# Performance work log

Hardware: AMD Instinct MI355X
Metric: run time of the kernel (lower is better)

## Reference

```python
import jax, jax.numpy as jnp
import numpy as np

D_MODEL = 1024
N_HEADS = 4  # hardcoded in the torch reshape
EPS = 1e-5


def setup_inputs() -> dict:
    key = jax.random.key(0)
    ks = jax.random.split(key, 5)
    d = D_MODEL
    x = jax.random.normal(ks[0], (4, 2048, d), dtype=jnp.float32)
    scale = 1.0 / np.sqrt(d)
    qkv_w = jax.random.normal(ks[1], (3 * d, d), dtype=jnp.float32) * scale
    qkv_b = jnp.zeros((3 * d,), dtype=jnp.float32)
    wo_w = jax.random.normal(ks[2], (d, d), dtype=jnp.float32) * scale
    wo_b = jnp.zeros((d,), dtype=jnp.float32)
    gamma = jnp.ones((d,), dtype=jnp.float32)
    beta = jnp.zeros((d,), dtype=jnp.float32)
    return {"x": x, "qkv_w": qkv_w, "qkv_b": qkv_b, "wo_w": wo_w,
            "wo_b": wo_b, "gamma": gamma, "beta": beta}


def reference(x, qkv_w, qkv_b, wo_w, wo_b, gamma, beta):
    b, s, d = x.shape
    h = N_HEADS
    hd = d // h
    # QKV projection (torch Linear: x @ W.T + b)
    qkv = x @ qkv_w.T + qkv_b                      # [b, s, 3d]
    qkv = qkv.reshape(b, s, 3, h, hd)
    qkv = jnp.transpose(qkv, (2, 0, 3, 1, 4))      # [3, b, h, s, hd]
    q, k, v = qkv[0], qkv[1], qkv[2]
    scores = jnp.einsum('bhqd,bhkd->bhqk', q, k) * (hd ** -0.5)
    attn = jax.nn.softmax(scores, axis=-1)
    out = jnp.einsum('bhqk,bhkd->bhqd', attn, v)   # [b, h, s, hd]
    out = jnp.transpose(out, (0, 2, 1, 3)).reshape(b, s, d)
    y = x + (out @ wo_w.T + wo_b)
    # LayerNorm over last dim
    mu = jnp.mean(y, axis=-1, keepdims=True)
    var = jnp.var(y, axis=-1, keepdims=True)
    return (y - mu) * jax.lax.rsqrt(var + EPS) * gamma + beta
```

## Files before the change

### kernel.cpp

```cpp
#include <hip/hip_runtime.h>
#include <hip/hip_bf16.h>

#define SEQ 2048
#define DM  1024
#define NH  4
#define HD  256

typedef __attribute__((ext_vector_type(4))) float f32x4;
typedef __attribute__((ext_vector_type(16))) float f32x16;
typedef __attribute__((ext_vector_type(8))) short bf16x8;

__device__ __forceinline__ void gload16(const void* g, void* l) {
  __builtin_amdgcn_global_load_lds(
      (__attribute__((address_space(1))) void*)(unsigned long long)(g),
      (__attribute__((address_space(3))) void*)(l), 16, 0, 0);
}

__device__ __forceinline__ bf16x8 ldg8(const __hip_bfloat16* p) {
  return *reinterpret_cast<const bf16x8*>(p);
}

__device__ __forceinline__ unsigned pack2(float a, float b) {
  __hip_bfloat162 t = __float22bfloat162_rn(make_float2(a, b));
  return *reinterpret_cast<unsigned*>(&t);
}

__device__ __forceinline__ short bfbits(float x) {
  __hip_bfloat16 h = __float2bfloat16(x);
  return *reinterpret_cast<short*>(&h);
}

__global__ __launch_bounds__(256) void cvt_f32_bf16(const float* __restrict__ in,
                                                    __hip_bfloat16* __restrict__ out, int n4) {
  int i = blockIdx.x * 256 + threadIdx.x;
  if (i >= n4) return;
  float4 v = reinterpret_cast<const float4*>(in)[i];
  __hip_bfloat162* o2 = reinterpret_cast<__hip_bfloat162*>(out);
  o2[i * 2 + 0] = __float22bfloat162_rn(make_float2(v.x, v.y));
  o2[i * 2 + 1] = __float22bfloat162_rn(make_float2(v.z, v.w));
}

template <int EPI>
__global__ __launch_bounds__(256, 2) void gemm_bt(
    const __hip_bfloat16* __restrict__ A, const __hip_bfloat16* __restrict__ Bw,
    const float* __restrict__ bias, const float* __restrict__ resid,
    __hip_bfloat16* __restrict__ Cb, float* __restrict__ Cf, int M, int N, int K) {
  __shared__ __hip_bfloat16 ldsA[128 * 32];
  __shared__ __hip_bfloat16 ldsB[128 * 32];
  const int t = threadIdx.x;
  const int w = t >> 6, l = t & 63;
  const int lg = l >> 4, li = l & 15;
  const int m0 = blockIdx.y * 128, n0 = blockIdx.x * 128;
  const int wm = (w >> 1) * 64, wn = (w & 1) * 64;
  const int c1 = t + 256;
  const __hip_bfloat16* gA0 = A + (size_t)(m0 + (t >> 2)) * K + (t & 3) * 8;
  const __hip_bfloat16* gA1 = A + (size_t)(m0 + (c1 >> 2)) * K + (c1 & 3) * 8;
  const __hip_bfloat16* gB0 = Bw + (size_t)(n0 + (t >> 2)) * K + (t & 3) * 8;
  const __hip_bfloat16* gB1 = Bw + (size_t)(n0 + (c1 >> 2)) * K + (c1 & 3) * 8;
  __hip_bfloat16* lA0 = ldsA + t * 8;
  __hip_bfloat16* lA1 = ldsA + c1 * 8;
  __hip_bfloat16* lB0 = ldsB + t * 8;
  __hip_bfloat16* lB1 = ldsB + c1 * 8;
  f32x4 acc[4][4] = {};
  for (int k0 = 0; k0 < K; k0 += 32) {
    gload16(gA0 + k0, lA0);
    gload16(gA1 + k0, lA1);
    gload16(gB0 + k0, lB0);
    gload16(gB1 + k0, lB1);
    __syncthreads();
    bf16x8 af[4], bfr[4];
#pragma unroll
    for (int i = 0; i < 4; i++) af[i] = ldg8(&ldsA[(wm + i * 16 + li) * 32 + lg * 8]);
#pragma unroll
    for (int i = 0; i < 4; i++) bfr[i] = ldg8(&ldsB[(wn + i * 16 + li) * 32 + lg * 8]);
#pragma unroll
    for (int mi = 0; mi < 4; mi++)
#pragma unroll
      for (int ni = 0; ni < 4; ni++)
        acc[mi][ni] = __builtin_amdgcn_mfma_f32_16x16x32_bf16(af[mi], bfr[ni], acc[mi][ni], 0, 0, 0);
    __syncthreads();
  }
#pragma unroll
  for (int ni = 0; ni < 4; ni++) {
    const int col = n0 + wn + ni * 16 + li;
    const float bv = bias[col];
#pragma unroll
    for (int mi = 0; mi < 4; mi++) {
      const int rowb = m0 + wm + mi * 16 + lg * 4;
#pragma unroll
      for (int r = 0; r < 4; r++) {
        const size_t idx = (size_t)(rowb + r) * N + col;
        float v = acc[mi][ni][r] + bv;
        if (EPI) {
          Cf[idx] = v + resid[idx];
        } else {
          Cb[idx] = __float2bfloat16(v);
        }
      }
    }
  }
}

__global__ __launch_bounds__(256) void transpose_v(const short* __restrict__ qkv,
                                                   short* __restrict__ vt) {
  __shared__ short tile[32][36];
  const int t = threadIdx.x;
  const int bh = blockIdx.z, b = bh >> 2, h = bh & 3;
  const int s0 = blockIdx.x * 32, d0 = blockIdx.y * 32;
  const int sr = t >> 3, c4 = (t & 7) * 4;
  const short* src = qkv + (size_t)(b * SEQ + s0 + sr) * 3072 + 2048 + h * HD + d0 + c4;
  short4 vv = *reinterpret_cast<const short4*>(src);
  tile[sr][c4 + 0] = vv.x;
  tile[sr][c4 + 1] = vv.y;
  tile[sr][c4 + 2] = vv.z;
  tile[sr][c4 + 3] = vv.w;
  __syncthreads();
  short* dst = vt + (size_t)(bh * HD + d0 + sr) * SEQ + s0 + c4;
  short4 ov;
  ov.x = tile[c4 + 0][sr];
  ov.y = tile[c4 + 1][sr];
  ov.z = tile[c4 + 2][sr];
  ov.w = tile[c4 + 3][sr];
  *reinterpret_cast<short4*>(dst) = ov;
}

__global__ __launch_bounds__(512, 2) void flash_attn(const __hip_bfloat16* __restrict__ qkv,
                                                     const __hip_bfloat16* __restrict__ vt,
                                                     __hip_bfloat16* __restrict__ attno) {
  __shared__ __hip_bfloat16 ldsK[2][2][32 * 256];
  __shared__ __hip_bfloat16 ldsV[2][2][256 * 32];
  __shared__ float mlx[8][2][32];
  const int tid = threadIdx.x, w = tid >> 6, l = tid & 63;
  const int l31 = l & 31, hi = l >> 5;
  const int g = w >> 2, gt = tid & 255;
  const int bid = blockIdx.x;
  const int bh = (bid & 7) * 2 + ((bid >> 3) & 1);
  const int qt = bid >> 4;
  const int b = bh >> 2, h = bh & 3;
  const int qsub = qt * 128 + (w & 3) * 32;
  const int kvbase = g * 1024;
  bf16x8 bq[16];
  {
    const __hip_bfloat16* Qp = qkv + (size_t)(b * SEQ + qsub + l31) * 3072 + h * HD + hi * 8;
#pragma unroll
    for (int kst = 0; kst < 16; kst++) bq[kst] = ldg8(Qp + kst * 16);
  }
  const int kcd = (gt & 31) ^ ((gt >> 5) & 7);
  const __hip_bfloat16* Kg =
      qkv + (size_t)(b * SEQ + kvbase + (gt >> 5)) * 3072 + 1024 + h * HD + kcd * 8;
  const int vcd = (gt & 3) ^ ((gt >> 3) & 3);
  const __hip_bfloat16* Vg =
      vt + (size_t)bh * HD * SEQ + (size_t)(gt >> 2) * SEQ + kvbase + vcd * 8;
  __hip_bfloat16* lKb[2] = {&ldsK[g][0][0], &ldsK[g][1][0]};
  __hip_bfloat16* lVb[2] = {&ldsV[g][0][0], &ldsV[g][1][0]};

  f32x16 oacc[8] = {};
  float m_run = -1e30f, lsum = 0.f;

#pragma unroll
  for (int i = 0; i < 4; i++) gload16(Kg + (size_t)(i * 8) * 3072, lKb[0] + i * 2048 + gt * 8);
#pragma unroll
  for (int i = 0; i < 4; i++) gload16(Vg + (size_t)(i * 64) * SEQ, lVb[0] + i * 2048 + gt * 8);
  __syncthreads();

#pragma unroll 2
  for (int t = 0; t < 32; ++t) {
    const int cur = t & 1;
    if (t + 1 < 32) {
      const int nk = (t + 1) * 32;
#pragma unroll
      for (int i = 0; i < 4; i++)
        gload16(Kg + (size_t)(nk + i * 8) * 3072, lKb[cur ^ 1] + i * 2048 + gt * 8);
#pragma unroll
      for (int i = 0; i < 4; i++)
        gload16(Vg + (size_t)(i * 64) * SEQ + nk, lVb[cur ^ 1] + i * 2048 + gt * 8);
    }
    const __hip_bfloat16* lK = lKb[cur];
    const __hip_bfloat16* lV = lVb[cur];
    f32x16 sa = {}, sb = {};
    const int ksw = l31 & 7;
    __builtin_amdgcn_s_setprio(1);
#pragma unroll
    for (int kst = 0; kst < 8; kst++) {
      bf16x8 aka = ldg8(&lK[l31 * 256 + (((4 * kst + hi) ^ ksw) << 3)]);
      bf16x8 akb = ldg8(&lK[l31 * 256 + (((4 * kst + 2 + hi) ^ ksw) << 3)]);
      sa = __builtin_amdgcn_mfma_f32_32x32x16_bf16(aka, bq[2 * kst], sa, 0, 0, 0);
      sb = __builtin_amdgcn_mfma_f32_32x32x16_bf16(akb, bq[2 * kst + 1], sb, 0, 0, 0);
    }
    __builtin_amdgcn_s_setprio(0);
#pragma unroll
    for (int r = 0; r < 16; r++) sa[r] = (sa[r] + sb[r]) * 0.0625f;
    float rmax = sa[0];
#pragma unroll
    for (int r = 1; r < 16; r++) rmax = fmaxf(rmax, sa[r]);
    rmax = fmaxf(rmax, __shfl_xor(rmax, 32));
    if (rmax > m_run + 8.f) {
      const float alpha = __expf(m_run - rmax);
      m_run = rmax;
      lsum *= alpha;
#pragma unroll
      for (int dt = 0; dt < 8; dt++)
#pragma unroll
        for (int r = 0; r < 16; r++) oacc[dt][r] *= alpha;
    }
    float psum = 0.f;
#pragma unroll
    for (int r = 0; r < 16; r++) {
      sa[r] = __expf(sa[r] - m_run);
      psum += sa[r];
    }
    lsum += psum + __shfl_xor(psum, 32);
#pragma unroll
    for (int ks = 0; ks < 2; ks++) {
      const int rb = ks * 8;
      unsigned a0 = pack2(sa[rb + 0], sa[rb + 1]);
      unsigned a1 = pack2(sa[rb + 2], sa[rb + 3]);
      unsigned b0 = pack2(sa[rb + 4], sa[rb + 5]);
      unsigned b1 = pack2(sa[rb + 6], sa[rb + 7]);
      unsigned s0 = (unsigned)__shfl_xor((int)(hi ? a0 : b0), 32);
      unsigned s1 = (unsigned)__shfl_xor((int)(hi ? a1 : b1), 32);
      union { unsigned u[4]; bf16x8 v; } pw;
      pw.u[0] = hi ? s0 : a0;
      pw.u[1] = hi ? s1 : a1;
      pw.u[2] = hi ? b0 : s0;
      pw.u[3] = hi ? b1 : s1;
      __builtin_amdgcn_s_setprio(1);
#pragma unroll
      for (int dt = 0; dt < 8; dt++) {
        const int drow = dt * 32 + l31;
        bf16x8 av = ldg8(&lV[drow * 32 + (((ks * 2 + hi) ^ ((drow >> 1) & 3)) << 3)]);
        oacc[dt] = __builtin_amdgcn_mfma_f32_32x32x16_bf16(av, pw.v, oacc[dt], 0, 0, 0);
      }
      __builtin_amdgcn_s_setprio(0);
    }
    __syncthreads();
  }
  if (l < 32) {
    mlx[w][0][l] = m_run;
    mlx[w][1][l] = lsum;
  }
  __syncthreads();
  {
    const float m_o = mlx[w ^ 4][0][l31];
    const float l_o = mlx[w ^ 4][1][l31];
    const float mm = fmaxf(m_run, m_o);
    const float e_s = __expf(m_run - mm), e_o = __expf(m_o - mm);
    const float wgt = e_s / (e_s * lsum + e_o * l_o);
#pragma unroll
    for (int dt = 0; dt < 8; dt++)
#pragma unroll
      for (int r = 0; r < 16; r++) oacc[dt][r] *= wgt;
  }
  const int pair = w & 3;
  float* xch = pair < 2 ? reinterpret_cast<float*>(&ldsK[0][0][0]) + pair * 8192
                        : reinterpret_cast<float*>(&ldsV[0][0][0]) + (pair - 2) * 8192;
  if (g == 0) {
#pragma unroll
    for (int dt = 0; dt < 8; dt++)
#pragma unroll
      for (int rq = 0; rq < 4; rq++) {
        const int dch = dt * 8 + 2 * rq + hi;
        f32x4 v;
#pragma unroll
        for (int i = 0; i < 4; i++) v[i] = oacc[dt][4 * rq + i];
        *reinterpret_cast<f32x4*>(&xch[l31 * 256 + ((dch ^ (l31 & 7)) << 2)]) = v;
      }
  }
  __syncthreads();
  if (g == 1) {
    const size_t rowb = (size_t)(b * SEQ + qsub + l31) * DM + h * HD;
#pragma unroll
    for (int dt = 0; dt < 8; dt++)
#pragma unroll
      for (int rq = 0; rq < 4; rq++) {
        const int dch = dt * 8 + 2 * rq + hi;
        f32x4 p = *reinterpret_cast<const f32x4*>(&xch[l31 * 256 + ((dch ^ (l31 & 7)) << 2)]);
        short4 sv;
        sv.x = bfbits(p[0] + oacc[dt][4 * rq + 0]);
        sv.y = bfbits(p[1] + oacc[dt][4 * rq + 1]);
        sv.z = bfbits(p[2] + oacc[dt][4 * rq + 2]);
        sv.w = bfbits(p[3] + oacc[dt][4 * rq + 3]);
        *reinterpret_cast<short4*>(
            reinterpret_cast<short*>(attno + rowb + dt * 32 + 8 * rq + 4 * hi)) = sv;
      }
  }
}

__global__ __launch_bounds__(256) void layernorm_k(const float* __restrict__ y,
                                                   const float* __restrict__ gamma,
                                                   const float* __restrict__ beta,
                                                   float* __restrict__ out) {
  const int w = threadIdx.x >> 6, l = threadIdx.x & 63;
  const size_t row = (size_t)blockIdx.x * 4 + w;
  const float4* yp = reinterpret_cast<const float4*>(y + row * DM);
  float4 v[4];
  float s = 0.f, s2 = 0.f;
#pragma unroll
  for (int i = 0; i < 4; i++) {
    v[i] = yp[i * 64 + l];
    s += v[i].x + v[i].y + v[i].z + v[i].w;
    s2 += v[i].x * v[i].x + v[i].y * v[i].y + v[i].z * v[i].z + v[i].w * v[i].w;
  }
#pragma unroll
  for (int off = 1; off < 64; off <<= 1) {
    s += __shfl_xor(s, off);
    s2 += __shfl_xor(s2, off);
  }
  const float mu = s * (1.f / 1024.f);
  const float rs = rsqrtf(s2 * (1.f / 1024.f) - mu * mu + 1e-5f);
  const float4* gp = reinterpret_cast<const float4*>(gamma);
  const float4* bp = reinterpret_cast<const float4*>(beta);
  float4* op = reinterpret_cast<float4*>(out + row * DM);
#pragma unroll
  for (int i = 0; i < 4; i++) {
    float4 g = gp[i * 64 + l], bb = bp[i * 64 + l];
    float4 o;
    o.x = (v[i].x - mu) * rs * g.x + bb.x;
    o.y = (v[i].y - mu) * rs * g.y + bb.y;
    o.z = (v[i].z - mu) * rs * g.z + bb.z;
    o.w = (v[i].w - mu) * rs * g.w + bb.w;
    op[i * 64 + l] = o;
  }
}

extern "C" void kernel_launch(void* const* d_in, const int* in_sizes, int n_in,
                              void* d_out, int out_size, void* d_ws, size_t ws_size,
                              hipStream_t stream) {
  const float* x     = (const float*)d_in[0];
  const float* qkv_w = (const float*)d_in[1];
  const float* qkv_b = (const float*)d_in[2];
  const float* wo_w  = (const float*)d_in[3];
  const float* wo_b  = (const float*)d_in[4];
  const float* gamma = (const float*)d_in[5];
  const float* beta  = (const float*)d_in[6];
  float* out = (float*)d_out;
  char* ws = (char*)d_ws;
  __hip_bfloat16* xbf   = (__hip_bfloat16*)(ws);
  __hip_bfloat16* qkvwb = (__hip_bfloat16*)(ws + 16777216);
  __hip_bfloat16* wowb  = (__hip_bfloat16*)(ws + 23068672);
  __hip_bfloat16* qkv   = (__hip_bfloat16*)(ws + 25165824);
  float*          yb    = (float*)(ws + 25165824);
  __hip_bfloat16* vt    = (__hip_bfloat16*)(ws + 75497472);
  __hip_bfloat16* attno = xbf;

  cvt_f32_bf16<<<8192, 256, 0, stream>>>(x, xbf, 2097152);
  cvt_f32_bf16<<<3072, 256, 0, stream>>>(qkv_w, qkvwb, 786432);
  cvt_f32_bf16<<<1024, 256, 0, stream>>>(wo_w, wowb, 262144);
  gemm_bt<0><<<dim3(24, 64), 256, 0, stream>>>(xbf, qkvwb, qkv_b, nullptr, qkv, nullptr,
                                               8192, 3072, 1024);
  transpose_v<<<dim3(64, 8, 16), 256, 0, stream>>>((const short*)qkv, (short*)vt);
  flash_attn<<<256, 512, 0, stream>>>(qkv, vt, attno);
  gemm_bt<1><<<dim3(8, 64), 256, 0, stream>>>(attno, wowb, wo_b, x, nullptr, yb,
                                              8192, 1024, 1024);
  layernorm_k<<<2048, 256, 0, stream>>>(yb, gamma, beta, out);
}
```

Measured before the change: 247.2 us.

## Triple-buffer GEMM LDS with swizzled layout and merge conversion kernels

The GEMM main loop now prefetches two K-tiles ahead into three LDS buffers. It uses explicit vmcnt waits and one barrier per iteration instead of two syncthreads, so global loads overlap MFMA work. The LDS layout is XOR-swizzled to cut bank conflicts on fragment reads, and launch bounds rise to 3 blocks per CU. The three fp32-to-bf16 conversion launches are merged into one kernel to save launch overhead. The risks are higher LDS use per block and reliance on hand-tuned wait counts being correct.

```diff
diff --git a/kernel.cpp b/kernel.cpp
--- a/kernel.cpp
+++ b/kernel.cpp
@@ -30,55 +30,95 @@
   return *reinterpret_cast<short*>(&h);
 }
 
-__global__ __launch_bounds__(256) void cvt_f32_bf16(const float* __restrict__ in,
-                                                    __hip_bfloat16* __restrict__ out, int n4) {
+__global__ __launch_bounds__(256) void cvt3(const float* __restrict__ x,
+                                            const float* __restrict__ qw,
+                                            const float* __restrict__ ww,
+                                            __hip_bfloat16* __restrict__ xo,
+                                            __hip_bfloat16* __restrict__ qo,
+                                            __hip_bfloat16* __restrict__ wo) {
   int i = blockIdx.x * 256 + threadIdx.x;
-  if (i >= n4) return;
-  float4 v = reinterpret_cast<const float4*>(in)[i];
-  __hip_bfloat162* o2 = reinterpret_cast<__hip_bfloat162*>(out);
-  o2[i * 2 + 0] = __float22bfloat162_rn(make_float2(v.x, v.y));
-  o2[i * 2 + 1] = __float22bfloat162_rn(make_float2(v.z, v.w));
+  const float* src;
+  __hip_bfloat16* dst;
+  int j;
+  if (i < 2097152) {
+    src = x; dst = xo; j = i;
+  } else if (i < 2883584) {
+    src = qw; dst = qo; j = i - 2097152;
+  } else {
+    src = ww; dst = wo; j = i - 2883584;
+  }
+  float4 v = reinterpret_cast<const float4*>(src)[j];
+  __hip_bfloat162* o2 = reinterpret_cast<__hip_bfloat162*>(dst);
+  o2[j * 2 + 0] = __float22bfloat162_rn(make_float2(v.x, v.y));
+  o2[j * 2 + 1] = __float22bfloat162_rn(make_float2(v.z, v.w));
 }
 
 template <int EPI>
-__global__ __launch_bounds__(256, 2) void gemm_bt(
+__global__ __launch_bounds__(256, 3) void gemm_bt(
     const __hip_bfloat16* __restrict__ A, const __hip_bfloat16* __restrict__ Bw,
     const float* __restrict__ bias, const float* __restrict__ resid,
     __hip_bfloat16* __restrict__ Cb, float* __restrict__ Cf, int M, int N, int K) {
-  __shared__ __hip_bfloat16 ldsA[128 * 32];
-  __shared__ __hip_bfloat16 ldsB[128 * 32];
+  __shared__ __hip_bfloat16 lA[3][128 * 32];
+  __shared__ __hip_bfloat16 lB[3][128 * 32];
   const int t = threadIdx.x;
   const int w = t >> 6, l = t & 63;
   const int lg = l >> 4, li = l & 15;
   const int m0 = blockIdx.y * 128, n0 = blockIdx.x * 128;
   const int wm = (w >> 1) * 64, wn = (w & 1) * 64;
-  const int c1 = t + 256;
-  const __hip_bfloat16* gA0 = A + (size_t)(m0 + (t >> 2)) * K + (t & 3) * 8;
-  const __hip_bfloat16* gA1 = A + (size_t)(m0 + (c1 >> 2)) * K + (c1 & 3) * 8;
-  const __hip_bfloat16* gB0 = Bw + (size_t)(n0 + (t >> 2)) * K + (t & 3) * 8;
-  const __hip_bfloat16* gB1 = Bw + (size_t)(n0 + (c1 >> 2)) * K + (c1 & 3) * 8;
-  __hip_bfloat16* lA0 = ldsA + t * 8;
-  __hip_bfloat16* lA1 = ldsA + c1 * 8;
-  __hip_bfloat16* lB0 = ldsB + t * 8;
-  __hip_bfloat16* lB1 = ldsB + c1 * 8;
+  const int ca = (((t & 3) ^ ((t >> 3) & 3))) * 8;
+  const __hip_bfloat16* gA0 = A + (size_t)(m0 + (t >> 2)) * K + ca;
+  const __hip_bfloat16* gA1 = A + (size_t)(m0 + 64 + (t >> 2)) * K + ca;
+  const __hip_bfloat16* gB0 = Bw + (size_t)(n0 + (t >> 2)) * K + ca;
+  const __hip_bfloat16* gB1 = Bw + (size_t)(n0 + 64 + (t >> 2)) * K + ca;
+  const int loff = t * 8;
+
+  auto STAGE = [&](int kt, int buf) {
+    const int k0 = kt * 32;
+    gload16(gA0 + k0, &lA[buf][loff]);
+    gload16(gA1 + k0, &lA[buf][loff + 2048]);
+    gload16(gB0 + k0, &lB[buf][loff]);
+    gload16(gB1 + k0, &lB[buf][loff + 2048]);
+  };
+
   f32x4 acc[4][4] = {};
-  for (int k0 = 0; k0 < K; k0 += 32) {
-    gload16(gA0 + k0, lA0);
-    gload16(gA1 + k0, lA1);
-    gload16(gB0 + k0, lB0);
-    gload16(gB1 + k0, lB1);
-    __syncthreads();
+  const int T = K >> 5;
+  STAGE(0, 0);
+  STAGE(1, 1);
+  asm volatile("s_waitcnt vmcnt(4)" ::: "memory");
+  __builtin_amdgcn_sched_barrier(0);
+  __builtin_amdgcn_s_barrier();
+  __builtin_amdgcn_sched_barrier(0);
+  int cur = 0, nx2 = 2;
+  for (int kt = 0; kt < T; ++kt) {
+    if (kt + 2 < T) STAGE(kt + 2, nx2);
     bf16x8 af[4], bfr[4];
 #pragma unroll
-    for (int i = 0; i < 4; i++) af[i] = ldg8(&ldsA[(wm + i * 16 + li) * 32 + lg * 8]);
-#pragma unroll
-    for (int i = 0; i < 4; i++) bfr[i] = ldg8(&ldsB[(wn + i * 16 + li) * 32 + lg * 8]);
+    for (int i = 0; i < 4; i++) {
+      const int row = wm + i * 16 + li;
+      af[i] = ldg8(&lA[cur][row * 32 + ((lg ^ ((row >> 1) & 3)) << 3)]);
+    }
+#pragma unroll
+    for (int i = 0; i < 4; i++) {
+      const int row = wn + i * 16 + li;
+      bfr[i] = ldg8(&lB[cur][row * 32 + ((lg ^ ((row >> 1) & 3)) << 3)]);
+    }
+    asm volatile("s_waitcnt lgkmcnt(0)" ::: "memory");
+    __builtin_amdgcn_sched_barrier(0);
 #pragma unroll
     for (int mi = 0; mi < 4; mi++)
 #pragma unroll
       for (int ni = 0; ni < 4; ni++)
         acc[mi][ni] = __builtin_amdgcn_mfma_f32_16x16x32_bf16(af[mi], bfr[ni], acc[mi][ni], 0, 0, 0);
-    __syncthreads();
+    if (kt + 2 < T) {
+      asm volatile("s_waitcnt vmcnt(4)" ::: "memory");
+    } else {
+      asm volatile("s_waitcnt vmcnt(0)" ::: "memory");
+    }
+    __builtin_amdgcn_sched_barrier(0);
+    __builtin_amdgcn_s_barrier();
+    __builtin_amdgcn_sched_barrier(0);
+    cur = (cur == 2) ? 0 : cur + 1;
+    nx2 = (nx2 == 2) ? 0 : nx2 + 1;
   }
 #pragma unroll
   for (int ni = 0; ni < 4; ni++) {
@@ -343,9 +383,7 @@
   __hip_bfloat16* vt    = (__hip_bfloat16*)(ws + 75497472);
   __hip_bfloat16* attno = xbf;
 
-  cvt_f32_bf16<<<8192, 256, 0, stream>>>(x, xbf, 2097152);
-  cvt_f32_bf16<<<3072, 256, 0, stream>>>(qkv_w, qkvwb, 786432);
-  cvt_f32_bf16<<<1024, 256, 0, stream>>>(wo_w, wowb, 262144);
+  cvt3<<<12288, 256, 0, stream>>>(x, qkv_w, wo_w, xbf, qkvwb, wowb);
   gemm_bt<0><<<dim3(24, 64), 256, 0, stream>>>(xbf, qkvwb, qkv_b, nullptr, qkv, nullptr,
                                                8192, 3072, 1024);
   transpose_v<<<dim3(64, 8, 16), 256, 0, stream>>>((const short*)qkv, (short*)vt);
```

Result: faster. 240.1 us (-2.9%).
